# Optimization experiments

Hardware: AMD Instinct MI355X
Metric: run time of the kernel (lower is better)

The kernel has to match this reference:

```python
import jax, jax.numpy as jnp
import numpy as np

B, S, D, H, HD = 8, 1, 4096, 32, 128
MAX_SEQ, AL, FF = 2048, 10, 11008
START_POS = 2047
EPS = 1e-5


def setup_inputs() -> dict:
    key = jax.random.key(0)
    ks = jax.random.split(key, 12)
    # real RoPE angles for the single decode position START_POS
    inv_freq = 1.0 / (10000.0 ** (np.arange(0, HD, 2, dtype=np.float32) / HD))  # [HD/2]
    ang = (np.float32(START_POS) * inv_freq)[None, :]  # [S=1, HD/2]
    return {
        "x": jax.random.normal(ks[0], (B, S, D), jnp.float32),
        "adapter": jax.random.normal(ks[1], (1, AL, D), jnp.float32),
        "cache_k": jax.random.normal(ks[2], (B, MAX_SEQ, H, HD), jnp.float32),
        "cache_v": jax.random.normal(ks[3], (B, MAX_SEQ, H, HD), jnp.float32),
        "freqs_cos": jnp.cos(jnp.asarray(ang)),
        "freqs_sin": jnp.sin(jnp.asarray(ang)),
        "wq": jax.random.normal(ks[4], (D, D), jnp.float32) * 0.02,
        "wk": jax.random.normal(ks[5], (D, D), jnp.float32) * 0.02,
        "wv": jax.random.normal(ks[6], (D, D), jnp.float32) * 0.02,
        "wo": jax.random.normal(ks[7], (D, D), jnp.float32) * 0.02,
        "gate": jax.random.normal(ks[8], (1, H, 1, 1), jnp.float32) * 0.5,
        "attn_norm_w": jnp.ones((D,), jnp.float32),
        "ffn_norm_w": jnp.ones((D,), jnp.float32),
        "w1": jax.random.normal(ks[9], (D, FF), jnp.float32) * 0.02,
        "w2": jax.random.normal(ks[10], (FF, D), jnp.float32) * 0.02,
        "w3": jax.random.normal(ks[11], (D, FF), jnp.float32) * 0.02,
        "start_pos": START_POS,
    }


def _rmsnorm(x, w, eps=EPS):
    xf = x.astype(jnp.float32)
    return (xf * jax.lax.rsqrt(jnp.mean(xf * xf, axis=-1, keepdims=True) + eps)).astype(x.dtype) * w


def _rope(t, cos, sin):
    # t: [B,S,H,HD]; pairs are interleaved as in view_as_complex(reshape(..,-1,2))
    tr = t.reshape(*t.shape[:-1], HD // 2, 2)
    a, b = tr[..., 0], tr[..., 1]
    c = cos[None, :, None, :]
    s = sin[None, :, None, :]
    out = jnp.stack([a * c - b * s, a * s + b * c], axis=-1)
    return out.reshape(t.shape)


def _sdpa(q, k, v):
    # q:[B,H,S,HD], k/v:[B,H,K,HD]
    scores = jnp.einsum("bhqd,bhkd->bhqk", q, k) / jnp.sqrt(jnp.float32(HD))
    p = jax.nn.softmax(scores.astype(jnp.float32), axis=-1).astype(q.dtype)
    return jnp.einsum("bhqk,bhkd->bhqd", p, v)


def reference(x, adapter, cache_k, cache_v, freqs_cos, freqs_sin,
              wq, wk, wv, wo, gate, attn_norm_w, ffn_norm_w, w1, w2, w3, start_pos):
    bsz, seqlen, _ = x.shape
    # --- attention sub-block ---
    xn = _rmsnorm(x, attn_norm_w)
    xq = (xn @ wq).reshape(bsz, seqlen, H, HD)
    xk = (xn @ wk).reshape(bsz, seqlen, H, HD)
    xv = (xn @ wv).reshape(bsz, seqlen, H, HD)
    xq = _rope(xq, freqs_cos, freqs_sin)
    xk = _rope(xk, freqs_cos, freqs_sin)
    # KV-cache append
    cache_k = jax.lax.dynamic_update_slice(cache_k, xk, (0, start_pos, 0, 0))
    cache_v = jax.lax.dynamic_update_slice(cache_v, xv, (0, start_pos, 0, 0))
    keys = cache_k[:, : start_pos + seqlen].transpose(0, 2, 1, 3)   # [B,H,K,HD]
    values = cache_v[:, : start_pos + seqlen].transpose(0, 2, 1, 3)
    q = xq.transpose(0, 2, 1, 3)                                     # [B,H,S,HD]
    out = _sdpa(q, keys, values)                                     # [B,H,S,HD]
    # adapter-gated cross attention (adapter keys/values: no RoPE, shared over batch)
    ak = (adapter @ wk).reshape(AL, H, HD).transpose(1, 0, 2)        # [H,AL,HD]
    av = (adapter @ wv).reshape(AL, H, HD).transpose(1, 0, 2)        # [H,AL,HD]
    a_scores = jnp.einsum("bhqd,hkd->bhqk", q, ak) / jnp.sqrt(jnp.float32(HD))
    a_p = jax.nn.softmax(a_scores.astype(jnp.float32), axis=-1).astype(q.dtype)
    a_out = jnp.einsum("bhqk,hkd->bhqd", a_p, av)
    out = out + jnp.tanh(gate) * a_out
    attn_out = out.transpose(0, 2, 1, 3).reshape(bsz, seqlen, H * HD) @ wo
    h = x + attn_out
    # --- feed-forward sub-block (SwiGLU) ---
    hn = _rmsnorm(h, ffn_norm_w)
    ffn = (jax.nn.silu(hn @ w1) * (hn @ w3)) @ w2
    return h + ffn
```

## Files before the change

### kernel.cpp

```cpp
#include <hip/hip_runtime.h>
#include <cmath>

#define D_ 4096
#define H_ 32
#define HD_ 128
#define B_ 8
#define MAXSEQ_ 2048
#define AL_ 10
#define FF_ 11008
#define SCALE_ 0.08838834764831845f
#define EPS_ 1e-5f

__global__ __launch_bounds__(256) void rmsnorm_k(const float* __restrict__ in,
                                                 const float* __restrict__ w,
                                                 float* __restrict__ out) {
  int b = blockIdx.x, tid = threadIdx.x;
  const float* x = in + (size_t)b * D_;
  float ss = 0.f;
  for (int i = tid; i < D_; i += 256) { float v = x[i]; ss += v * v; }
  __shared__ float red[256];
  red[tid] = ss; __syncthreads();
  for (int s = 128; s; s >>= 1) { if (tid < s) red[tid] += red[tid + s]; __syncthreads(); }
  float r = rsqrtf(red[0] / (float)D_ + EPS_);
  float* o = out + (size_t)b * D_;
  for (int i = tid; i < D_; i += 256) o[i] = x[i] * r * w[i];
}

__global__ void copy_k(const float* __restrict__ in, float* __restrict__ out, int n) {
  int i = blockIdx.x * 256 + threadIdx.x;
  if (i < n) out[i] = in[i];
}

template<int ROWS, int CHUNK>
__global__ __launch_bounds__(256) void gemv_atomic(
    const float* __restrict__ X,
    const float* __restrict__ Wa, const float* __restrict__ Wb, const float* __restrict__ Wc,
    float* __restrict__ Ya, float* __restrict__ Yb, float* __restrict__ Yc,
    int N, int K) {
  constexpr int RS = (ROWS + 3) & ~3;
  const float* W = (blockIdx.z == 0) ? Wa : (blockIdx.z == 1) ? Wb : Wc;
  float*       Y = (blockIdx.z == 0) ? Ya : (blockIdx.z == 1) ? Yb : Yc;
  __shared__ float xs[CHUNK][RS];
  int tid = threadIdx.x;
  int i0 = blockIdx.y * CHUNK;
  for (int idx = tid; idx < ROWS * CHUNK; idx += 256) {
    int r = idx / CHUNK, ii = idx - r * CHUNK;
    xs[ii][r] = X[(size_t)r * K + i0 + ii];
  }
  __syncthreads();
  int N2 = N >> 1;
  int j2 = blockIdx.x * 256 + tid;
  if (j2 >= N2) return;
  float2 acc[ROWS];
#pragma unroll
  for (int r = 0; r < ROWS; ++r) acc[r] = make_float2(0.f, 0.f);
  const float2* W2 = (const float2*)W;
  for (int ii = 0; ii < CHUNK; ++ii) {
    float2 w = W2[(size_t)(i0 + ii) * N2 + j2];
    float xr[RS];
#pragma unroll
    for (int q = 0; q < RS / 4; ++q)
      *(float4*)&xr[4 * q] = *(const float4*)&xs[ii][4 * q];
#pragma unroll
    for (int r = 0; r < ROWS; ++r) { acc[r].x += xr[r] * w.x; acc[r].y += xr[r] * w.y; }
  }
#pragma unroll
  for (int r = 0; r < ROWS; ++r) {
    atomicAdd(&Y[(size_t)r * N + 2 * j2],     acc[r].x);
    atomicAdd(&Y[(size_t)r * N + 2 * j2 + 1], acc[r].y);
  }
}

__global__ void rope_k(float* __restrict__ qp, float* __restrict__ kp,
                       const float* __restrict__ fc, const float* __restrict__ fs) {
  int tid = blockIdx.x * 256 + threadIdx.x;
  if (tid >= 32768) return;
  float* buf = (tid & 16384) ? kp : qp;
  int p = tid & 16383;
  int b = p >> 11;
  int rem = p & 2047;
  int h = rem >> 6, i = rem & 63;
  size_t base = (size_t)b * D_ + h * HD_ + 2 * i;
  float a = buf[base], bb = buf[base + 1];
  float c = fc[i], s = fs[i];
  buf[base]     = a * c - bb * s;
  buf[base + 1] = a * s + bb * c;
}

__global__ __launch_bounds__(256) void attn_partial(
    const float* __restrict__ qp,
    const float* __restrict__ kp,
    const float* __restrict__ vp,
    const float* __restrict__ ck,
    const float* __restrict__ cv,
    float* __restrict__ part) {
  int idx = blockIdx.x;
  int c = idx & 7, bh = idx >> 3;
  int h = bh & 31, b = bh >> 5;
  int tid = threadIdx.x, wave = tid >> 6, lane = tid & 63;
  __shared__ float sc[256];
  __shared__ float red[256];
  __shared__ float ob[4][128];
  int t0 = c * 256;
  float2 qv = *(const float2*)&qp[(size_t)b * D_ + h * HD_ + 2 * lane];
  for (int k = 0; k < 64; ++k) {
    int tl = wave * 64 + k;
    int t = t0 + tl;
    const float* kptr = (t == MAXSEQ_ - 1)
        ? &kp[(size_t)b * D_ + h * HD_]
        : &ck[(((size_t)b * MAXSEQ_ + t) * H_ + h) * HD_];
    float2 kv = *(const float2*)&kptr[2 * lane];
    float s = qv.x * kv.x + qv.y * kv.y;
    for (int off = 32; off; off >>= 1) s += __shfl_xor(s, off);
    if (lane == 0) sc[tl] = s * SCALE_;
  }
  __syncthreads();
  float sv = sc[tid];
  red[tid] = sv; __syncthreads();
  for (int s = 128; s; s >>= 1) { if (tid < s) red[tid] = fmaxf(red[tid], red[tid + s]); __syncthreads(); }
  float m = red[0]; __syncthreads();
  float p = __expf(sv - m);
  sc[tid] = p;
  red[tid] = p; __syncthreads();
  for (int s = 128; s; s >>= 1) { if (tid < s) red[tid] += red[tid + s]; __syncthreads(); }
  float l = red[0];
  float2 acc = make_float2(0.f, 0.f);
  for (int tl = wave; tl < 256; tl += 4) {
    int t = t0 + tl;
    const float* vptr = (t == MAXSEQ_ - 1)
        ? &vp[(size_t)b * D_ + h * HD_]
        : &cv[(((size_t)b * MAXSEQ_ + t) * H_ + h) * HD_];
    float2 vv = *(const float2*)&vptr[2 * lane];
    float pp = sc[tl];
    acc.x += pp * vv.x; acc.y += pp * vv.y;
  }
  ob[wave][2 * lane] = acc.x;
  ob[wave][2 * lane + 1] = acc.y;
  __syncthreads();
  float* po = &part[(size_t)idx * 132];
  if (tid == 0) { po[0] = m; po[1] = l; }
  if (tid < 128) po[4 + tid] = ob[0][tid] + ob[1][tid] + ob[2][tid] + ob[3][tid];
}

__global__ __launch_bounds__(128) void attn_combine(
    const float* __restrict__ part,
    const float* __restrict__ qp,
    const float* __restrict__ kvk,
    const float* __restrict__ kvv,
    const float* __restrict__ gate,
    float* __restrict__ attn) {
  int bh = blockIdx.x;
  int h = bh & 31, b = bh >> 5;
  int tid = threadIdx.x;
  const float* pb = &part[(size_t)bh * 8 * 132];
  float mc[8], lc[8];
  float M = -INFINITY;
  for (int c = 0; c < 8; ++c) { mc[c] = pb[c * 132]; lc[c] = pb[c * 132 + 1]; M = fmaxf(M, mc[c]); }
  float L = 0.f, O = 0.f;
  for (int c = 0; c < 8; ++c) {
    float e = __expf(mc[c] - M);
    L += e * lc[c];
    O += e * pb[c * 132 + 4 + tid];
  }
  float main_out = O / L;
  float qd = qp[(size_t)b * D_ + h * HD_ + tid];
  __shared__ float red[128];
  __shared__ float sa[10];
  for (int j = 0; j < 10; ++j) {
    float prod = qd * kvk[(size_t)(8 + j) * D_ + h * HD_ + tid];
    red[tid] = prod; __syncthreads();
    for (int s = 64; s; s >>= 1) { if (tid < s) red[tid] += red[tid + s]; __syncthreads(); }
    if (tid == 0) sa[j] = red[0] * SCALE_;
    __syncthreads();
  }
  float ma = -INFINITY;
  for (int j = 0; j < 10; ++j) ma = fmaxf(ma, sa[j]);
  float la = 0.f, pj[10];
  for (int j = 0; j < 10; ++j) { pj[j] = __expf(sa[j] - ma); la += pj[j]; }
  float ao = 0.f;
  for (int j = 0; j < 10; ++j) ao += pj[j] * kvv[(size_t)(8 + j) * D_ + h * HD_ + tid];
  ao /= la;
  float g = tanhf(gate[h]);
  attn[(size_t)b * D_ + h * HD_ + tid] = main_out + g * ao;
}

__global__ void silu_mul_k(const float* __restrict__ g1, const float* __restrict__ g3,
                           float* __restrict__ g, int n) {
  int i = blockIdx.x * 256 + threadIdx.x;
  if (i < n) { float a = g1[i]; g[i] = (a / (1.f + __expf(-a))) * g3[i]; }
}

extern "C" void kernel_launch(void* const* d_in, const int* in_sizes, int n_in,
                              void* d_out, int out_size, void* d_ws, size_t ws_size,
                              hipStream_t stream) {
  (void)in_sizes; (void)n_in; (void)out_size; (void)ws_size;
  const float* x       = (const float*)d_in[0];
  const float* adapter = (const float*)d_in[1];
  const float* ck      = (const float*)d_in[2];
  const float* cv      = (const float*)d_in[3];
  const float* fc      = (const float*)d_in[4];
  const float* fs      = (const float*)d_in[5];
  const float* wq      = (const float*)d_in[6];
  const float* wk      = (const float*)d_in[7];
  const float* wv      = (const float*)d_in[8];
  const float* wo      = (const float*)d_in[9];
  const float* gate    = (const float*)d_in[10];
  const float* anw     = (const float*)d_in[11];
  const float* fnw     = (const float*)d_in[12];
  const float* w1      = (const float*)d_in[13];
  const float* w2      = (const float*)d_in[14];
  const float* w3      = (const float*)d_in[15];
  float* out = (float*)d_out;

  float* ws   = (float*)d_ws;
  float* xa   = ws;
  float* qp   = xa + 18 * D_;
  float* kp   = qp + 18 * D_;
  float* vp   = kp + 18 * D_;
  float* part = vp + 18 * D_;
  float* attn = part + 2048 * 132;
  float* hbuf = attn + 8 * D_;
  float* hn   = hbuf + 8 * D_;
  float* g1   = hn + 8 * D_;
  float* g3b  = g1 + 8 * FF_;
  float* gb   = g3b + 8 * FF_;

  rmsnorm_k<<<8, 256, 0, stream>>>(x, anw, xa);
  copy_k<<<(AL_ * D_ + 255) / 256, 256, 0, stream>>>(adapter, xa + 8 * D_, AL_ * D_);
  hipMemsetAsync(qp, 0, (size_t)3 * 18 * D_ * sizeof(float), stream);
  gemv_atomic<18, 256><<<dim3(8, 16, 3), 256, 0, stream>>>(xa, wq, wk, wv, qp, kp, vp, D_, D_);
  rope_k<<<128, 256, 0, stream>>>(qp, kp, fc, fs);
  attn_partial<<<2048, 256, 0, stream>>>(qp, kp, vp, ck, cv, part);
  attn_combine<<<256, 128, 0, stream>>>(part, qp, kp, vp, gate, attn);
  copy_k<<<128, 256, 0, stream>>>(x, hbuf, 8 * D_);
  gemv_atomic<8, 128><<<dim3(8, 32, 1), 256, 0, stream>>>(attn, wo, wo, wo, hbuf, hbuf, hbuf, D_, D_);
  rmsnorm_k<<<8, 256, 0, stream>>>(hbuf, fnw, hn);
  hipMemsetAsync(g1, 0, (size_t)2 * 8 * FF_ * sizeof(float), stream);
  gemv_atomic<8, 256><<<dim3(22, 16, 2), 256, 0, stream>>>(hn, w1, w3, w3, g1, g3b, g3b, FF_, D_);
  silu_mul_k<<<(8 * FF_ + 255) / 256, 256, 0, stream>>>(g1, g3b, gb, 8 * FF_);
  copy_k<<<128, 256, 0, stream>>>(hbuf, out, 8 * D_);
  gemv_atomic<8, 256><<<dim3(8, 43, 1), 256, 0, stream>>>(gb, w2, w2, w2, out, out, out, D_, FF_);
}
```

Before: 410.2 us.

## Vectorize GEMV and attention loads to float4, fuse copies, use unsafe atomics

GEMV threads now each handle four output columns with float4 weight loads, and the K-chunk and grid shapes are retuned to keep enough blocks in flight. The attention partial kernel puts two keys per wave, each read with float4 loads by 32 lanes. Residual and adapter copies are folded into neighbouring kernels to remove launches. atomicAdd is replaced with unsafeAtomicAdd to allow hardware float atomics. The aim is to cut launch overhead and improve weight-streaming bandwidth, at the cost of more registers per thread and more atomic traffic from the smaller K chunks.

```diff
diff --git a/kernel.cpp b/kernel.cpp
--- a/kernel.cpp
+++ b/kernel.cpp
@@ -10,6 +10,29 @@
 #define FF_ 11008
 #define SCALE_ 0.08838834764831845f
 #define EPS_ 1e-5f
+
+__global__ __launch_bounds__(256) void norm_adapter_k(const float* __restrict__ x,
+                                                      const float* __restrict__ w,
+                                                      const float* __restrict__ adapter,
+                                                      float* __restrict__ xa) {
+  int b = blockIdx.x, tid = threadIdx.x;
+  if (b < 8) {
+    const float* xr = x + (size_t)b * D_;
+    float ss = 0.f;
+    for (int i = tid; i < D_; i += 256) { float v = xr[i]; ss += v * v; }
+    __shared__ float red[256];
+    red[tid] = ss; __syncthreads();
+    for (int s = 128; s; s >>= 1) { if (tid < s) red[tid] += red[tid + s]; __syncthreads(); }
+    float r = rsqrtf(red[0] / (float)D_ + EPS_);
+    float* o = xa + (size_t)b * D_;
+    for (int i = tid; i < D_; i += 256) o[i] = xr[i] * r * w[i];
+  } else {
+    int r = b - 8;
+    const float4* src = (const float4*)(adapter + (size_t)r * D_);
+    float4* dst = (float4*)(xa + (size_t)(8 + r) * D_);
+    for (int i = tid; i < D_ / 4; i += 256) dst[i] = src[i];
+  }
+}
 
 __global__ __launch_bounds__(256) void rmsnorm_k(const float* __restrict__ in,
                                                  const float* __restrict__ w,
@@ -24,11 +47,6 @@
   float r = rsqrtf(red[0] / (float)D_ + EPS_);
   float* o = out + (size_t)b * D_;
   for (int i = tid; i < D_; i += 256) o[i] = x[i] * r * w[i];
-}
-
-__global__ void copy_k(const float* __restrict__ in, float* __restrict__ out, int n) {
-  int i = blockIdx.x * 256 + threadIdx.x;
-  if (i < n) out[i] = in[i];
 }
 
 template<int ROWS, int CHUNK>
@@ -48,26 +66,32 @@
     xs[ii][r] = X[(size_t)r * K + i0 + ii];
   }
   __syncthreads();
-  int N2 = N >> 1;
-  int j2 = blockIdx.x * 256 + tid;
-  if (j2 >= N2) return;
-  float2 acc[ROWS];
-#pragma unroll
-  for (int r = 0; r < ROWS; ++r) acc[r] = make_float2(0.f, 0.f);
-  const float2* W2 = (const float2*)W;
+  int N4 = N >> 2;
+  int j4 = blockIdx.x * 256 + tid;
+  if (j4 >= N4) return;
+  float4 acc[ROWS];
+#pragma unroll
+  for (int r = 0; r < ROWS; ++r) acc[r] = make_float4(0.f, 0.f, 0.f, 0.f);
+  const float4* W4 = (const float4*)W;
   for (int ii = 0; ii < CHUNK; ++ii) {
-    float2 w = W2[(size_t)(i0 + ii) * N2 + j2];
+    float4 w = W4[(size_t)(i0 + ii) * N4 + j4];
     float xr[RS];
 #pragma unroll
     for (int q = 0; q < RS / 4; ++q)
       *(float4*)&xr[4 * q] = *(const float4*)&xs[ii][4 * q];
 #pragma unroll
-    for (int r = 0; r < ROWS; ++r) { acc[r].x += xr[r] * w.x; acc[r].y += xr[r] * w.y; }
+    for (int r = 0; r < ROWS; ++r) {
+      acc[r].x += xr[r] * w.x; acc[r].y += xr[r] * w.y;
+      acc[r].z += xr[r] * w.z; acc[r].w += xr[r] * w.w;
+    }
   }
 #pragma unroll
   for (int r = 0; r < ROWS; ++r) {
-    atomicAdd(&Y[(size_t)r * N + 2 * j2],     acc[r].x);
-    atomicAdd(&Y[(size_t)r * N + 2 * j2 + 1], acc[r].y);
+    float* yp = &Y[(size_t)r * N + 4 * j4];
+    unsafeAtomicAdd(yp + 0, acc[r].x);
+    unsafeAtomicAdd(yp + 1, acc[r].y);
+    unsafeAtomicAdd(yp + 2, acc[r].z);
+    unsafeAtomicAdd(yp + 3, acc[r].w);
   }
 }
 
@@ -98,21 +122,23 @@
   int c = idx & 7, bh = idx >> 3;
   int h = bh & 31, b = bh >> 5;
   int tid = threadIdx.x, wave = tid >> 6, lane = tid & 63;
+  int half = lane >> 5, l32 = lane & 31;
   __shared__ float sc[256];
   __shared__ float red[256];
   __shared__ float ob[4][128];
   int t0 = c * 256;
-  float2 qv = *(const float2*)&qp[(size_t)b * D_ + h * HD_ + 2 * lane];
-  for (int k = 0; k < 64; ++k) {
-    int tl = wave * 64 + k;
+  const float4 qv = *(const float4*)&qp[(size_t)b * D_ + h * HD_ + 4 * l32];
+  for (int i = 0; i < 32; ++i) {
+    int tl = wave * 64 + 2 * i + half;
     int t = t0 + tl;
     const float* kptr = (t == MAXSEQ_ - 1)
         ? &kp[(size_t)b * D_ + h * HD_]
         : &ck[(((size_t)b * MAXSEQ_ + t) * H_ + h) * HD_];
-    float2 kv = *(const float2*)&kptr[2 * lane];
-    float s = qv.x * kv.x + qv.y * kv.y;
-    for (int off = 32; off; off >>= 1) s += __shfl_xor(s, off);
-    if (lane == 0) sc[tl] = s * SCALE_;
+    float4 kv = *(const float4*)&kptr[4 * l32];
+    float s = qv.x * kv.x + qv.y * kv.y + qv.z * kv.z + qv.w * kv.w;
+    s += __shfl_xor(s, 16); s += __shfl_xor(s, 8);
+    s += __shfl_xor(s, 4);  s += __shfl_xor(s, 2); s += __shfl_xor(s, 1);
+    if (l32 == 0) sc[tl] = s * SCALE_;
   }
   __syncthreads();
   float sv = sc[tid];
@@ -124,18 +150,23 @@
   red[tid] = p; __syncthreads();
   for (int s = 128; s; s >>= 1) { if (tid < s) red[tid] += red[tid + s]; __syncthreads(); }
   float l = red[0];
-  float2 acc = make_float2(0.f, 0.f);
-  for (int tl = wave; tl < 256; tl += 4) {
+  float4 acc = make_float4(0.f, 0.f, 0.f, 0.f);
+  for (int i = 0; i < 32; ++i) {
+    int tl = wave * 64 + 2 * i + half;
     int t = t0 + tl;
     const float* vptr = (t == MAXSEQ_ - 1)
         ? &vp[(size_t)b * D_ + h * HD_]
         : &cv[(((size_t)b * MAXSEQ_ + t) * H_ + h) * HD_];
-    float2 vv = *(const float2*)&vptr[2 * lane];
+    float4 vv = *(const float4*)&vptr[4 * l32];
     float pp = sc[tl];
-    acc.x += pp * vv.x; acc.y += pp * vv.y;
-  }
-  ob[wave][2 * lane] = acc.x;
-  ob[wave][2 * lane + 1] = acc.y;
+    acc.x += pp * vv.x; acc.y += pp * vv.y; acc.z += pp * vv.z; acc.w += pp * vv.w;
+  }
+  acc.x += __shfl_xor(acc.x, 32); acc.y += __shfl_xor(acc.y, 32);
+  acc.z += __shfl_xor(acc.z, 32); acc.w += __shfl_xor(acc.w, 32);
+  if (half == 0) {
+    ob[wave][4 * l32 + 0] = acc.x; ob[wave][4 * l32 + 1] = acc.y;
+    ob[wave][4 * l32 + 2] = acc.z; ob[wave][4 * l32 + 3] = acc.w;
+  }
   __syncthreads();
   float* po = &part[(size_t)idx * 132];
   if (tid == 0) { po[0] = m; po[1] = l; }
@@ -148,7 +179,9 @@
     const float* __restrict__ kvk,
     const float* __restrict__ kvv,
     const float* __restrict__ gate,
-    float* __restrict__ attn) {
+    const float* __restrict__ x,
+    float* __restrict__ attn,
+    float* __restrict__ hbuf) {
   int bh = blockIdx.x;
   int h = bh & 31, b = bh >> 5;
   int tid = threadIdx.x;
@@ -181,13 +214,17 @@
   for (int j = 0; j < 10; ++j) ao += pj[j] * kvv[(size_t)(8 + j) * D_ + h * HD_ + tid];
   ao /= la;
   float g = tanhf(gate[h]);
-  attn[(size_t)b * D_ + h * HD_ + tid] = main_out + g * ao;
-}
-
-__global__ void silu_mul_k(const float* __restrict__ g1, const float* __restrict__ g3,
-                           float* __restrict__ g, int n) {
+  size_t oidx = (size_t)b * D_ + h * HD_ + tid;
+  attn[oidx] = main_out + g * ao;
+  hbuf[oidx] = x[oidx];
+}
+
+__global__ void silu_out_k(const float* __restrict__ g1, const float* __restrict__ g3,
+                           float* __restrict__ g, const float* __restrict__ hbuf,
+                           float* __restrict__ out, int n) {
   int i = blockIdx.x * 256 + threadIdx.x;
   if (i < n) { float a = g1[i]; g[i] = (a / (1.f + __expf(-a))) * g3[i]; }
+  if (i < 8 * D_) out[i] = hbuf[i];
 }
 
 extern "C" void kernel_launch(void* const* d_in, const int* in_sizes, int n_in,
@@ -225,19 +262,16 @@
   float* g3b  = g1 + 8 * FF_;
   float* gb   = g3b + 8 * FF_;
 
-  rmsnorm_k<<<8, 256, 0, stream>>>(x, anw, xa);
-  copy_k<<<(AL_ * D_ + 255) / 256, 256, 0, stream>>>(adapter, xa + 8 * D_, AL_ * D_);
+  norm_adapter_k<<<18, 256, 0, stream>>>(x, anw, adapter, xa);
   hipMemsetAsync(qp, 0, (size_t)3 * 18 * D_ * sizeof(float), stream);
-  gemv_atomic<18, 256><<<dim3(8, 16, 3), 256, 0, stream>>>(xa, wq, wk, wv, qp, kp, vp, D_, D_);
+  gemv_atomic<18, 128><<<dim3(4, 32, 3), 256, 0, stream>>>(xa, wq, wk, wv, qp, kp, vp, D_, D_);
   rope_k<<<128, 256, 0, stream>>>(qp, kp, fc, fs);
   attn_partial<<<2048, 256, 0, stream>>>(qp, kp, vp, ck, cv, part);
-  attn_combine<<<256, 128, 0, stream>>>(part, qp, kp, vp, gate, attn);
-  copy_k<<<128, 256, 0, stream>>>(x, hbuf, 8 * D_);
-  gemv_atomic<8, 128><<<dim3(8, 32, 1), 256, 0, stream>>>(attn, wo, wo, wo, hbuf, hbuf, hbuf, D_, D_);
+  attn_combine<<<256, 128, 0, stream>>>(part, qp, kp, vp, gate, x, attn, hbuf);
+  gemv_atomic<8, 64><<<dim3(4, 64, 1), 256, 0, stream>>>(attn, wo, wo, wo, hbuf, hbuf, hbuf, D_, D_);
   rmsnorm_k<<<8, 256, 0, stream>>>(hbuf, fnw, hn);
   hipMemsetAsync(g1, 0, (size_t)2 * 8 * FF_ * sizeof(float), stream);
-  gemv_atomic<8, 256><<<dim3(22, 16, 2), 256, 0, stream>>>(hn, w1, w3, w3, g1, g3b, g3b, FF_, D_);
-  silu_mul_k<<<(8 * FF_ + 255) / 256, 256, 0, stream>>>(g1, g3b, gb, 8 * FF_);
-  copy_k<<<128, 256, 0, stream>>>(hbuf, out, 8 * D_);
-  gemv_atomic<8, 256><<<dim3(8, 43, 1), 256, 0, stream>>>(gb, w2, w2, w2, out, out, out, D_, FF_);
-}
+  gemv_atomic<8, 128><<<dim3(11, 32, 2), 256, 0, stream>>>(hn, w1, w3, w3, g1, g3b, g3b, FF_, D_);
+  silu_out_k<<<(8 * FF_ + 255) / 256, 256, 0, stream>>>(g1, g3b, gb, hbuf, out, 8 * FF_);
+  gemv_atomic<8, 86><<<dim3(4, 128, 1), 256, 0, stream>>>(gb, w2, w2, w2, out, out, out, D_, FF_);
+}
```

Result: slower. 622.3 us (+51.7%).
